# Performance work log

Hardware: AMD Instinct MI355X
Metric: run time of the kernel (lower is better)

Reference implementation:

```python
import jax, jax.numpy as jnp
import numpy as np

N, M, D = 8192, 8192, 256

def setup_inputs() -> dict:
    key = jax.random.key(0)
    k1, k2, k3, k4 = jax.random.split(key, 4)
    x1 = jax.random.normal(k1, (N, D), dtype=jnp.float32)
    x2 = jax.random.normal(k2, (M, D), dtype=jnp.float32)
    alpha_raw = jax.random.normal(k3, (D,), dtype=jnp.float32)      # nn.Parameter(torch.randn(input_dim))
    variance_raw = jnp.ones((1,), dtype=jnp.float32)                # nn.Parameter(torch.ones(1))
    return {"x1": x1, "x2": x2, "alpha_raw": alpha_raw, "variance_raw": variance_raw}

def reference(x1, x2, alpha_raw, variance_raw):
    # alpha = softmax(alpha_raw^2), variance = variance_raw^2
    alpha = jax.nn.softmax(alpha_raw ** 2)                          # (D,)
    variance = variance_raw ** 2                                    # (1,)
    # GEMM rewrite of sum_d alpha_d (x1_i - x2_j)^2:
    #   ||x1*sqrt(a)||^2 - 2 (x1*sqrt(a))(x2*sqrt(a))^T + ||x2*sqrt(a)||^2
    sa = jnp.sqrt(alpha)
    a = x1 * sa                                                     # (N, D)
    b = x2 * sa                                                     # (M, D)
    sq = (jnp.sum(a * a, axis=-1)[:, None]
          - 2.0 * (a @ b.T)
          + jnp.sum(b * b, axis=-1)[None, :])                       # (N, M)
    sq = jnp.maximum(sq, 0.0)  # numerical guard; exact value is non-negative
    kernel = variance * jnp.exp(-0.5 * sq)                          # (N, M)
    if kernel.shape[0] == 1:
        kernel = jnp.squeeze(kernel)
    return kernel
```

## Files before the change

### kernel.cpp

```cpp
#include <hip/hip_runtime.h>
#include <stdint.h>

#define NROWS 8192
#define MCOLS 8192
#define KDIM  256

typedef __bf16 bf16x8 __attribute__((ext_vector_type(8)));
typedef float  floatx4 __attribute__((ext_vector_type(4)));
typedef unsigned short ushort4v __attribute__((ext_vector_type(4)));

__device__ __forceinline__ unsigned short f32_to_bf16_rne(float f) {
    unsigned int u = __float_as_uint(f);
    u += 0x7FFFu + ((u >> 16) & 1u);
    return (unsigned short)(u >> 16);
}
__device__ __forceinline__ float bf16_to_f32(unsigned short h) {
    return __uint_as_float(((unsigned int)h) << 16);
}

__device__ __forceinline__ void async16(const void* g, void* l) {
    __builtin_amdgcn_global_load_lds(
        (const __attribute__((address_space(1))) unsigned int*)g,
        (__attribute__((address_space(3))) unsigned int*)l,
        16, 0, 0);
}

__global__ void prep_rows(const float* __restrict__ x1, const float* __restrict__ x2,
                          const float* __restrict__ araw,
                          unsigned short* __restrict__ Amat, unsigned short* __restrict__ Bmat,
                          float* __restrict__ ra, float* __restrict__ rb) {
    __shared__ float sa_lds[256];
    __shared__ float wred[8];
    int tid  = threadIdx.x;
    int wave = tid >> 6;
    int lane = tid & 63;

    float z = araw[tid];
    z = z * z;
    float m = z;
#pragma unroll
    for (int off = 32; off; off >>= 1) m = fmaxf(m, __shfl_xor(m, off));
    if (lane == 0) wred[wave] = m;
    __syncthreads();
    float mx = fmaxf(fmaxf(wred[0], wred[1]), fmaxf(wred[2], wred[3]));
    float e = __expf(z - mx);
    float s = e;
#pragma unroll
    for (int off = 32; off; off >>= 1) s += __shfl_xor(s, off);
    if (lane == 0) wred[4 + wave] = s;
    __syncthreads();
    float sum = wred[4] + wred[5] + wred[6] + wred[7];
    sa_lds[tid] = sqrtf(e / sum);
    __syncthreads();

    int grow = blockIdx.x * 4 + wave;
    const float* x; unsigned short* mat; float* nrm; int row;
    if (grow < NROWS) { x = x1; mat = Amat; nrm = ra; row = grow; }
    else              { x = x2; mat = Bmat; nrm = rb; row = grow - NROWS; }

    floatx4 v  = *(const floatx4*)&x[(size_t)row * KDIM + lane * 4];
    floatx4 sv = *(const floatx4*)&sa_lds[lane * 4];
    ushort4v h;
    float p = 0.0f;
#pragma unroll
    for (int j = 0; j < 4; ++j) {
        float f = v[j] * sv[j];
        unsigned short hh = f32_to_bf16_rne(f);
        h[j] = hh;
        float fv = bf16_to_f32(hh);
        p += fv * fv;
    }
    *(ushort4v*)&mat[(size_t)row * KDIM + lane * 4] = h;
#pragma unroll
    for (int off = 32; off; off >>= 1) p += __shfl_xor(p, off);
    if (lane == 0) nrm[row] = p;
}

__global__ __launch_bounds__(256, 4) void rbf_gemm(
    const unsigned short* __restrict__ A, const unsigned short* __restrict__ B,
    const float* __restrict__ ra, const float* __restrict__ rb,
    const float* __restrict__ vraw, float* __restrict__ out)
{
    __shared__ unsigned short As[128 * 64];
    __shared__ unsigned short Bs[128 * 64];

    const int tid  = threadIdx.x;
    const int lane = tid & 63;
    const int wave = tid >> 6;

    const int wm = (wave & 1) * 64;
    const int wn = (wave >> 1) * 64;
    const int quad = lane >> 4;
    const int l15  = lane & 15;

    int bmv[2], bnv[2];
#pragma unroll
    for (int tt = 0; tt < 2; ++tt) {
        int g   = blockIdx.x + tt * 2048;
        int xcd = g & 7;
        int i   = g >> 3;
        bmv[tt] = (xcd >> 2) * 32 + (i >> 4);
        bnv[tt] = (xcd & 3) * 16 + (i & 15);
    }

    auto stage = [&](int bm, int bn, int k0) {
#pragma unroll
        for (int it = 0; it < 4; ++it) {
            int c   = it * 256 + tid;
            int row = c >> 3;
            int kc  = c & 7;
            int gkc = kc ^ (row & 7);
            const unsigned short* gA = A + (size_t)(bm * 128 + row) * KDIM + k0 + gkc * 8;
            const unsigned short* gB = B + (size_t)(bn * 128 + row) * KDIM + k0 + gkc * 8;
            async16(gA, &As[c * 8]);
            async16(gB, &Bs[c * 8]);
        }
    };

    const float variance = vraw[0] * vraw[0];

    stage(bmv[0], bnv[0], 0);

#pragma unroll
    for (int tt = 0; tt < 2; ++tt) {
        const int bm = bmv[tt];
        const int bn = bnv[tt];

        floatx4 acc[4][4];
#pragma unroll
        for (int tj = 0; tj < 4; tj++)
#pragma unroll
            for (int ti = 0; ti < 4; ti++) acc[tj][ti] = (floatx4)0.0f;

#pragma unroll
        for (int t = 0; t < 4; ++t) {
            __syncthreads();
#pragma unroll
            for (int ks = 0; ks < 2; ++ks) {
                bf16x8 af[4], bfr[4];
                int kc = ks * 4 + quad;
#pragma unroll
                for (int x = 0; x < 4; ++x) {
                    int mm  = wm + x * 16 + l15;
                    int sA  = mm * 8 + (kc ^ (mm & 7));
                    af[x]   = *(const bf16x8*)&As[sA * 8];
                    int nn  = wn + x * 16 + l15;
                    int sB  = nn * 8 + (kc ^ (nn & 7));
                    bfr[x]  = *(const bf16x8*)&Bs[sB * 8];
                }
#pragma unroll
                for (int tj = 0; tj < 4; ++tj)
#pragma unroll
                    for (int ti = 0; ti < 4; ++ti)
                        acc[tj][ti] = __builtin_amdgcn_mfma_f32_16x16x32_bf16(
                            bfr[tj], af[ti], acc[tj][ti], 0, 0, 0);
            }
            if (!(tt == 1 && t == 3)) {
                __syncthreads();
                if (t < 3)            stage(bm, bn, (t + 1) * 64);
                else                  stage(bmv[1], bnv[1], 0);
            }
        }

#pragma unroll
        for (int ti = 0; ti < 4; ++ti) {
            int row = bm * 128 + wm + ti * 16 + l15;
            float rav = ra[row];
            float* orow = out + (size_t)row * MCOLS;
#pragma unroll
            for (int tj = 0; tj < 4; ++tj) {
                int nbase = bn * 128 + wn + tj * 16 + quad * 4;
                floatx4 rbv = *(const floatx4*)&rb[nbase];
                floatx4 val;
#pragma unroll
                for (int r = 0; r < 4; ++r) {
                    float s = rav + rbv[r] - 2.0f * acc[tj][ti][r];
                    s = fmaxf(s, 0.0f);
                    val[r] = variance * __expf(-0.5f * s);
                }
                *(floatx4*)&orow[nbase] = val;
            }
        }
    }
}

extern "C" void kernel_launch(void* const* d_in, const int* in_sizes, int n_in,
                              void* d_out, int out_size, void* d_ws, size_t ws_size,
                              hipStream_t stream) {
    const float* x1   = (const float*)d_in[0];
    const float* x2   = (const float*)d_in[1];
    const float* araw = (const float*)d_in[2];
    const float* vraw = (const float*)d_in[3];
    float* out = (float*)d_out;

    char* ws = (char*)d_ws;
    float* ra = (float*)(ws + 1024);
    float* rb = (float*)(ws + 1024 + 32768);
    unsigned short* Amat = (unsigned short*)(ws + 66560);
    unsigned short* Bmat = (unsigned short*)(ws + 66560 + (size_t)NROWS * KDIM * 2);

    prep_rows<<<(NROWS + MCOLS) / 4, 256, 0, stream>>>(x1, x2, araw, Amat, Bmat, ra, rb);

    rbf_gemm<<<2048, 256, 0, stream>>>(Amat, Bmat, ra, rb, vraw, out);
}
```

Measured before the change: 339.5 us.

## Launch one output tile per block instead of two sequential tiles

The GEMM kernel previously processed two 128x128 output tiles per block, prefetching the next tile's first K-slice during the epilogue. Now the grid covers all 4096 tiles, with one tile per block and a simple stage-sync-compute loop. This gives the scheduler more blocks and removes the cross-tile prefetch, so the previous overlap of loading the second tile with the first tile's compute and epilogue is lost. Global loads are no longer overlapped with MFMA inside a block, and the kernel now relies on other resident blocks to hide that latency.

```diff
diff --git a/kernel.cpp b/kernel.cpp
--- a/kernel.cpp
+++ b/kernel.cpp
@@ -88,22 +88,25 @@
     const int lane = tid & 63;
     const int wave = tid >> 6;
 
+    const int g   = blockIdx.y * gridDim.x + blockIdx.x;
+    const int xcd = g & 7;
+    const int i   = g >> 3;
+    const int bm  = (xcd >> 2) * 32 + (i >> 4);
+    const int bn  = (xcd & 3) * 16 + (i & 15);
+
     const int wm = (wave & 1) * 64;
     const int wn = (wave >> 1) * 64;
     const int quad = lane >> 4;
     const int l15  = lane & 15;
 
-    int bmv[2], bnv[2];
+    floatx4 acc[4][4];
 #pragma unroll
-    for (int tt = 0; tt < 2; ++tt) {
-        int g   = blockIdx.x + tt * 2048;
-        int xcd = g & 7;
-        int i   = g >> 3;
-        bmv[tt] = (xcd >> 2) * 32 + (i >> 4);
-        bnv[tt] = (xcd & 3) * 16 + (i & 15);
-    }
+    for (int tj = 0; tj < 4; tj++)
+#pragma unroll
+        for (int ti = 0; ti < 4; ti++) acc[tj][ti] = (floatx4)0.0f;
 
-    auto stage = [&](int bm, int bn, int k0) {
+    for (int t = 0; t < 4; ++t) {
+        int k0 = t * 64;
 #pragma unroll
         for (int it = 0; it < 4; ++it) {
             int c   = it * 256 + tid;
@@ -115,71 +118,49 @@
             async16(gA, &As[c * 8]);
             async16(gB, &Bs[c * 8]);
         }
-    };
-
-    const float variance = vraw[0] * vraw[0];
-
-    stage(bmv[0], bnv[0], 0);
+        __syncthreads();
 
 #pragma unroll
-    for (int tt = 0; tt < 2; ++tt) {
-        const int bm = bmv[tt];
-        const int bn = bnv[tt];
+        for (int ks = 0; ks < 2; ++ks) {
+            bf16x8 af[4], bfr[4];
+            int kc = ks * 4 + quad;
+#pragma unroll
+            for (int x = 0; x < 4; ++x) {
+                int mm  = wm + x * 16 + l15;
+                int sA  = mm * 8 + (kc ^ (mm & 7));
+                af[x]   = *(const bf16x8*)&As[sA * 8];
+                int nn  = wn + x * 16 + l15;
+                int sB  = nn * 8 + (kc ^ (nn & 7));
+                bfr[x]  = *(const bf16x8*)&Bs[sB * 8];
+            }
+#pragma unroll
+            for (int tj = 0; tj < 4; ++tj)
+#pragma unroll
+                for (int ti = 0; ti < 4; ++ti)
+                    acc[tj][ti] = __builtin_amdgcn_mfma_f32_16x16x32_bf16(
+                        bfr[tj], af[ti], acc[tj][ti], 0, 0, 0);
+        }
+        if (t < 3) __syncthreads();
+    }
 
-        floatx4 acc[4][4];
+    float variance = vraw[0] * vraw[0];
 #pragma unroll
-        for (int tj = 0; tj < 4; tj++)
+    for (int ti = 0; ti < 4; ++ti) {
+        int row = bm * 128 + wm + ti * 16 + l15;
+        float rav = ra[row];
+        float* orow = out + (size_t)row * MCOLS;
 #pragma unroll
-            for (int ti = 0; ti < 4; ti++) acc[tj][ti] = (floatx4)0.0f;
-
+        for (int tj = 0; tj < 4; ++tj) {
+            int nbase = bn * 128 + wn + tj * 16 + quad * 4;
+            floatx4 rbv = *(const floatx4*)&rb[nbase];
+            floatx4 val;
 #pragma unroll
-        for (int t = 0; t < 4; ++t) {
-            __syncthreads();
-#pragma unroll
-            for (int ks = 0; ks < 2; ++ks) {
-                bf16x8 af[4], bfr[4];
-                int kc = ks * 4 + quad;
-#pragma unroll
-                for (int x = 0; x < 4; ++x) {
-                    int mm  = wm + x * 16 + l15;
-                    int sA  = mm * 8 + (kc ^ (mm & 7));
-                    af[x]   = *(const bf16x8*)&As[sA * 8];
-                    int nn  = wn + x * 16 + l15;
-                    int sB  = nn * 8 + (kc ^ (nn & 7));
-                    bfr[x]  = *(const bf16x8*)&Bs[sB * 8];
-                }
-#pragma unroll
-                for (int tj = 0; tj < 4; ++tj)
-#pragma unroll
-                    for (int ti = 0; ti < 4; ++ti)
-                        acc[tj][ti] = __builtin_amdgcn_mfma_f32_16x16x32_bf16(
-                            bfr[tj], af[ti], acc[tj][ti], 0, 0, 0);
+            for (int r = 0; r < 4; ++r) {
+                float s = rav + rbv[r] - 2.0f * acc[tj][ti][r];
+                s = fmaxf(s, 0.0f);
+                val[r] = variance * __expf(-0.5f * s);
             }
-            if (!(tt == 1 && t == 3)) {
-                __syncthreads();
-                if (t < 3)            stage(bm, bn, (t + 1) * 64);
-                else                  stage(bmv[1], bnv[1], 0);
-            }
-        }
-
-#pragma unroll
-        for (int ti = 0; ti < 4; ++ti) {
-            int row = bm * 128 + wm + ti * 16 + l15;
-            float rav = ra[row];
-            float* orow = out + (size_t)row * MCOLS;
-#pragma unroll
-            for (int tj = 0; tj < 4; ++tj) {
-                int nbase = bn * 128 + wn + tj * 16 + quad * 4;
-                floatx4 rbv = *(const floatx4*)&rb[nbase];
-                floatx4 val;
-#pragma unroll
-                for (int r = 0; r < 4; ++r) {
-                    float s = rav + rbv[r] - 2.0f * acc[tj][ti][r];
-                    s = fmaxf(s, 0.0f);
-                    val[r] = variance * __expf(-0.5f * s);
-                }
-                *(floatx4*)&orow[nbase] = val;
-            }
+            *(floatx4*)&orow[nbase] = val;
         }
     }
 }
@@ -201,5 +182,6 @@
 
     prep_rows<<<(NROWS + MCOLS) / 4, 256, 0, stream>>>(x1, x2, araw, Amat, Bmat, ra, rb);
 
-    rbf_gemm<<<2048, 256, 0, stream>>>(Amat, Bmat, ra, rb, vraw, out);
+    dim3 grid(MCOLS / 128, NROWS / 128);
+    rbf_gemm<<<grid, 256, 0, stream>>>(Amat, Bmat, ra, rb, vraw, out);
 }
```

Result: no change. 338.7 us (-0.2%).
